# Optimization experiments

Hardware: AMD Instinct MI355X
Metric: run time of the kernel (lower is better)

## Reference

```python
import jax, jax.numpy as jnp
import numpy as np

B, S, E, H = 2, 2048, 1024, 16
D = E // H          # head_dim = 64
HK = H // 4         # heads per kernel group = 4
MASKED_BIAS = -10000.0


def _dwconv_causal(x, w, b):
    # x: [B, h, S, D], w: [D, k], b: [D]; causal depthwise conv along S
    k = w.shape[1]
    s = x.shape[2]
    xp = jnp.pad(x, ((0, 0), (0, 0), (k - 1, 0), (0, 0)))
    out = b
    for i in range(k):
        out = out + xp[:, :, i:i + s, :] * w[:, i]
    return out


def setup_inputs() -> dict:
    key = jax.random.key(0)
    ks = jax.random.split(key, 32)
    inp = {
        'hidden_states': jax.random.normal(ks[0], (B, S, E), jnp.float32),
        'c_attn_w': jax.random.normal(ks[1], (E, 3 * E), jnp.float32) * 0.02,
        'c_attn_b': jnp.zeros((3 * E,), jnp.float32),
        'c_proj_w': jax.random.normal(ks[2], (E, E), jnp.float32) * 0.02,
        'c_proj_b': jnp.zeros((E,), jnp.float32),
    }
    i = 3
    for pre in ('q', 'k', 'v'):
        for kern in (3, 5, 7):
            inp[f'{pre}w{kern}'] = jax.random.normal(ks[i], (D, kern), jnp.float32) * (1.0 / kern)
            inp[f'{pre}b{kern}'] = jnp.zeros((D,), jnp.float32)
            i += 1
    return inp


def _forward(hidden_states, c_attn_w, c_attn_b, c_proj_w, c_proj_b,
             qw3, qb3, qw5, qb5, qw7, qb7,
             kw3, kb3, kw5, kb5, kw7, kb7,
             vw3, vb3, vw5, vb5, vw7, vb7):
    qkv = hidden_states @ c_attn_w + c_attn_b            # [B,S,3E]
    q, k, v = jnp.split(qkv, 3, axis=-1)

    def split_heads(t):
        return t.reshape(B, S, H, D).transpose(0, 2, 1, 3)  # [B,H,S,D]

    q, k, v = split_heads(q), split_heads(k), split_heads(v)

    def tranception_mix(t, ws_bs):
        parts = [t[:, :HK]]
        for g, (w, b) in enumerate(ws_bs):
            parts.append(_dwconv_causal(t[:, (g + 1) * HK:(g + 2) * HK], w, b))
        return jnp.concatenate(parts, axis=1)

    q = tranception_mix(q, [(qw3, qb3), (qw5, qb5), (qw7, qb7)])
    k = tranception_mix(k, [(kw3, kb3), (kw5, kb5), (kw7, kb7)])
    v = tranception_mix(v, [(vw3, vb3), (vw5, vb5), (vw7, vb7)])

    scores = jnp.einsum('bhqd,bhkd->bhqk', q, k) / jnp.sqrt(jnp.float32(D))
    causal = jnp.tril(jnp.ones((S, S), bool))
    scores = jnp.where(causal, scores, jnp.float32(MASKED_BIAS))
    attn = jax.nn.softmax(scores, axis=-1)
    out = jnp.einsum('bhqk,bhkd->bhqd', attn, v)
    out = out.transpose(0, 2, 1, 3).reshape(B, S, E)
    return out @ c_proj_w + c_proj_b


def reference(hidden_states, c_attn_w, c_attn_b, c_proj_w, c_proj_b,
              qw3, qb3, qw5, qb5, qw7, qb7,
              kw3, kb3, kw5, kb5, kw7, kb7,
              vw3, vb3, vw5, vb5, vw7, vb7):
    return _forward(hidden_states, c_attn_w, c_attn_b, c_proj_w, c_proj_b,
                    qw3, qb3, qw5, qb5, qw7, qb7,
                    kw3, kb3, kw5, kb5, kw7, kb7,
                    vw3, vb3, vw5, vb5, vw7, vb7)
```

## Files before the change

### kernel.cpp

```cpp
#include <hip/hip_runtime.h>
#include <stdint.h>
#include <math.h>

typedef unsigned short u16;
typedef __attribute__((ext_vector_type(8))) short short8;
typedef __attribute__((ext_vector_type(4))) float floatx4;

#define DEV static __device__ __forceinline__

struct alignas(8) us4 { u16 x, y, z, w; };
struct alignas(16) us8 { u16 v[8]; };
struct alignas(16) f4 { float x, y, z, w; };
struct alignas(8) f2 { float x, y; };
struct alignas(8) u32x2 { uint32_t x, y; };

DEV u16 f2bf(float f) {
  uint32_t u = __float_as_uint(f);
  u += 0x7fffu + ((u >> 16) & 1u);
  return (u16)(u >> 16);
}
DEV float bf2f(u16 h) { return __uint_as_float(((uint32_t)h) << 16); }

DEV uint32_t pkbf(float a, float b) {
#if __has_builtin(__builtin_amdgcn_cvt_pk_bf16_f32)
  typedef __attribute__((ext_vector_type(2))) __bf16 bf2_t;
  bf2_t v = __builtin_amdgcn_cvt_pk_bf16_f32(a, b);
  uint32_t r; __builtin_memcpy(&r, &v, 4); return r;
#else
  return (uint32_t)f2bf(a) | ((uint32_t)f2bf(b) << 16);
#endif
}

DEV float fexp2(float x) {
#if __has_builtin(__builtin_amdgcn_exp2f)
  return __builtin_amdgcn_exp2f(x);
#else
  return exp2f(x);
#endif
}

DEV void load_lds16(const void* g, void* l) {
  __builtin_amdgcn_global_load_lds((const __attribute__((address_space(1))) void*)g,
                                   (__attribute__((address_space(3))) void*)l, 16, 0, 0);
}

__global__ __launch_bounds__(256) void prep_fused(const float* __restrict__ hidden, u16* __restrict__ h_bf,
                                                  const float* __restrict__ attn_w, u16* __restrict__ wqkvT,
                                                  const float* __restrict__ proj_w, u16* __restrict__ wprojT) {
  __shared__ float tile[32][33];
  const int bx = blockIdx.x;
  const int t = threadIdx.x;
  if (bx < 4096) {
    const int i = (bx * 256 + t) * 4;
    f4 v = *(const f4*)(hidden + i);
    us4 o; o.x = f2bf(v.x); o.y = f2bf(v.y); o.z = f2bf(v.z); o.w = f2bf(v.w);
    *(us4*)(h_bf + i) = o;
    return;
  }
  const float* in; u16* out; int K, N, n0, k0;
  if (bx < 7168) {
    const int bid = bx - 4096;
    in = attn_w; out = wqkvT; K = 1024; N = 3072;
    n0 = (bid % 96) * 32; k0 = (bid / 96) * 32;
  } else {
    const int bid = bx - 7168;
    in = proj_w; out = wprojT; K = 1024; N = 1024;
    n0 = (bid & 31) * 32; k0 = (bid >> 5) * 32;
  }
  const int tx = t & 31, ty = t >> 5;
  for (int i = ty; i < 32; i += 8)
    tile[i][tx] = in[(size_t)(k0 + i) * N + n0 + tx];
  __syncthreads();
  for (int i = ty; i < 32; i += 8)
    out[(size_t)(n0 + i) * K + k0 + tx] = f2bf(tile[tx][i]);
}

template <int EPI, int BN, int NGRP>
__global__ __launch_bounds__(256) void gemm_bt(const u16* __restrict__ A,
                                               const u16* __restrict__ Bt,
                                               const float* __restrict__ bias,
                                               void* __restrict__ outp,
                                               int M, int N, int K) {
  constexpr int NT = BN / 32;
  __shared__ u16 lA[128 * 64];
  __shared__ u16 lB[BN * 64];
  const int t = threadIdx.x;
  const int w = t >> 6, lane = t & 63;
  const int quad = lane >> 4, l15 = lane & 15;
  const int wm = w >> 1, wn = w & 1;
  const int wn_off = wn * (BN / 2);

  const int bid = blockIdx.x;
  const int gsz = 32 * NGRP;
  const int grp = bid / gsz;
  const int r = bid - grp * gsz;
  const int m0 = (r & 31) * 128;
  const int n0 = (grp * NGRP + (r >> 5)) * BN;

  floatx4 acc[4][NT] = {};

  const int srow = t >> 3;
  const int scol = (((t & 7) ^ (srow & 7)) << 3);
  const u16* gA = A + (size_t)(m0 + srow) * K + scol;
  const u16* gB = Bt + (size_t)(n0 + srow) * K + scol;
  u16* sA = lA + t * 8;
  u16* sB = lB + t * 8;
  const size_t rstep = (size_t)32 * K;

  for (int k0 = 0; k0 < K; k0 += 64) {
#pragma unroll
    for (int c = 0; c < 4; c++) load_lds16(gA + c * rstep, sA + c * 2048);
#pragma unroll
    for (int c = 0; c < BN / 32; c++) load_lds16(gB + c * rstep, sB + c * 2048);
    gA += 64; gB += 64;
    __syncthreads();
#pragma unroll
    for (int kc = 0; kc < 2; kc++) {
      short8 af[4], bfr[NT];
#pragma unroll
      for (int mt = 0; mt < 4; mt++)
        af[mt] = *(const short8*)&lA[(wm * 64 + mt * 16 + l15) * 64 + (((kc * 4 + quad) ^ (l15 & 7)) << 3)];
#pragma unroll
      for (int nt = 0; nt < NT; nt++)
        bfr[nt] = *(const short8*)&lB[(wn_off + nt * 16 + l15) * 64 + (((kc * 4 + quad) ^ (l15 & 7)) << 3)];
#pragma unroll
      for (int mt = 0; mt < 4; mt++)
#pragma unroll
        for (int nt = 0; nt < NT; nt++)
          acc[mt][nt] = __builtin_amdgcn_mfma_f32_16x16x32_bf16(bfr[nt], af[mt], acc[mt][nt], 0, 0, 0);
    }
    __syncthreads();
  }

  if (EPI == 0) {
    u16* outq = (u16*)outp;
#pragma unroll
    for (int nt = 0; nt < NT; nt++) {
      const int nb = n0 + wn_off + nt * 16 + quad * 4;
      const f4 bn4 = *(const f4*)&bias[nb];
      const int tensor = nb >> 10, e = nb & 1023;
      const int h = e >> 6, d = e & 63;
      const size_t abase = (size_t)tensor * 4194304 + (size_t)h * 131072 + d;
#pragma unroll
      for (int mt = 0; mt < 4; mt++) {
        const int rr = m0 + wm * 64 + mt * 16 + l15;
        const int b = rr >> 11, s = rr & 2047;
        u32x2 o;
        o.x = pkbf(acc[mt][nt][0] + bn4.x, acc[mt][nt][1] + bn4.y);
        o.y = pkbf(acc[mt][nt][2] + bn4.z, acc[mt][nt][3] + bn4.w);
        *(u32x2*)&outq[abase + (size_t)b * 2097152 + (size_t)s * 64] = o;
      }
    }
  } else {
    float* outf = (float*)outp;
#pragma unroll
    for (int nt = 0; nt < NT; nt++) {
      const int nb = n0 + wn_off + nt * 16 + quad * 4;
      const f4 bn4 = *(const f4*)&bias[nb];
#pragma unroll
      for (int mt = 0; mt < 4; mt++) {
        const int rr = m0 + wm * 64 + mt * 16 + l15;
        f4 o;
        o.x = acc[mt][nt][0] + bn4.x;
        o.y = acc[mt][nt][1] + bn4.y;
        o.z = acc[mt][nt][2] + bn4.z;
        o.w = acc[mt][nt][3] + bn4.w;
        *(f4*)&outf[(size_t)rr * N + nb] = o;
      }
    }
  }
}

struct ConvW { const float* w[9]; const float* b[9]; };

template <int K>
DEV void conv_run(const u16* xt, int sl0, int d, const float* wp, const float* bp,
                  float qscale, float* out32) {
  float wr[K];
#pragma unroll
  for (int j = 0; j < K; j++) wr[j] = wp[d * K + j];
  const float br = bp[d];
  float win[K];
#pragma unroll
  for (int m = 1; m < K; m++) win[m] = bf2f(xt[(sl0 + 6 - K + m) * 68 + d]);
#pragma unroll
  for (int i = 0; i < 32; i++) {
#pragma unroll
    for (int m = 0; m < K - 1; m++) win[m] = win[m + 1];
    win[K - 1] = bf2f(xt[(sl0 + 6 + i) * 68 + d]);
    float val = br;
#pragma unroll
    for (int j = 0; j < K; j++) val += wr[j] * win[j];
    out32[i] = val * qscale;
  }
}

__global__ __launch_bounds__(256) void conv_mix(const u16* __restrict__ qkv, ConvW cw,
                                                u16* __restrict__ qpost,
                                                u16* __restrict__ kpost,
                                                u16* __restrict__ vpostT) {
  __shared__ u16 xt[134 * 68];
  __shared__ u16 yt[64 * 136];
  const int t = threadIdx.x;
  const int s0 = blockIdx.x * 128;
  const int h = blockIdx.y;
  const int tz = blockIdx.z;
  const int tensor = tz >> 1, b = tz & 1;
  const u16* src = qkv + (((size_t)tensor * 2 + b) * 16 + h) * 131072;

  for (int idx = t; idx < 134 * 16; idx += 256) {
    const int row = idx >> 4, c4 = (idx & 15) << 2;
    const int s = s0 - 6 + row;
    us4 v = {0, 0, 0, 0};
    if (s >= 0) v = *(const us4*)&src[(size_t)s * 64 + c4];
    *(us4*)&xt[row * 68 + c4] = v;
  }
  __syncthreads();

  const int group = h >> 2;
  const float* wp = (group > 0) ? cw.w[tensor * 3 + group - 1] : nullptr;
  const float* bp = (group > 0) ? cw.b[tensor * 3 + group - 1] : nullptr;
  const float qscale = (tensor == 0) ? 0.18033688f : 1.0f;

  const int d = t & 63;
  const int sl0 = (t >> 6) * 32;

  float out32[32];
  if (group == 0) {
#pragma unroll
    for (int i = 0; i < 32; i++)
      out32[i] = bf2f(xt[(sl0 + 6 + i) * 68 + d]) * qscale;
  } else if (group == 1) {
    conv_run<3>(xt, sl0, d, wp, bp, qscale, out32);
  } else if (group == 2) {
    conv_run<5>(xt, sl0, d, wp, bp, qscale, out32);
  } else {
    conv_run<7>(xt, sl0, d, wp, bp, qscale, out32);
  }

  if (tensor < 2) {
    u16* outp = (tensor == 0) ? qpost : kpost;
    const size_t ob = (((size_t)b * 16 + h) * 2048 + s0) * 64;
#pragma unroll
    for (int i = 0; i < 32; i++)
      outp[ob + (size_t)(sl0 + i) * 64 + d] = f2bf(out32[i]);
  } else {
#pragma unroll
    for (int i = 0; i < 32; i++)
      yt[d * 136 + sl0 + i] = f2bf(out32[i]);
    __syncthreads();
    const size_t ob = ((size_t)b * 16 + h) * 64;
    const int sl = (t & 15) * 8;
#pragma unroll
    for (int pass = 0; pass < 4; pass++) {
      const int dd = (t >> 4) + pass * 16;
      us8 vv = *(const us8*)&yt[dd * 136 + sl];
      *(us8*)&vpostT[(ob + dd) * 2048 + s0 + sl] = vv;
    }
  }
}

static __device__ const unsigned char kOrder[24] = {
  7, 8, 10, 12, 14, 16, 18, 20, 22, 23,
  6, 21, 5, 19, 4, 17, 3, 15, 2, 13, 1, 11, 0, 9
};

__global__ __launch_bounds__(256) void attn_fwd(const u16* __restrict__ Q,
                                                const u16* __restrict__ Kp,
                                                const u16* __restrict__ Vt,
                                                u16* __restrict__ Out,
                                                u16* __restrict__ Opart,
                                                float* __restrict__ lpart) {
  __shared__ u16 lK[2][128 * 64];
  __shared__ u16 lV[2][64 * 128];
  __shared__ u16 lP[4][32 * 64];
  const int t = threadIdx.x;
  const int w = t >> 6, lane = t & 63;
  const int quad = lane >> 4, l15 = lane & 15;
  const int e7 = l15 & 7;

  const int lin = blockIdx.x;
  const int xcd = lin & 7;
  const int rest = lin >> 3;
  const int grp = rest / 24;
  const int slot = kOrder[rest - grp * 24];
  const int bh = grp * 8 + xcd;

  int qi, jbeg, jend, split, half;
  if (slot < 8) {
    qi = slot; jbeg = 0; jend = qi + 1; split = 0; half = 0;
  } else {
    const int k = slot - 8;
    qi = 8 + (k >> 1); half = k & 1;
    jbeg = half ? 8 : 0; jend = half ? qi + 1 : 8; split = 1;
  }

  const int b = bh >> 4, h = bh & 15;
  const size_t qkbase = (size_t)bh * 131072;
  const int qblk = qi * 128 + w * 32;

  const int krow = t >> 3;
  const int kcol = (((t & 7) ^ (krow & 7)) << 3);
  const u16* gK = Kp + qkbase + (size_t)krow * 64 + kcol;
  const int vrow = t >> 4;
  const int vcol = (((t & 15) ^ vrow) << 3);
  const u16* gV = Vt + qkbase + (size_t)vrow * 2048 + vcol;
  u16* myP = lP[w];

  short8 qf[2][2];
#pragma unroll
  for (int qt = 0; qt < 2; qt++)
#pragma unroll
    for (int kc = 0; kc < 2; kc++)
      qf[qt][kc] = *(const short8*)&Q[qkbase + (size_t)(qblk + qt * 16 + l15) * 64 + kc * 32 + quad * 8];

  {
    const int j0 = jbeg * 128;
    u16* sK = &lK[0][0] + t * 8;
    u16* sV = &lV[0][0] + t * 8;
#pragma unroll
    for (int c = 0; c < 4; c++) {
      load_lds16(gK + (size_t)(j0 + c * 32) * 64, sK + c * 2048);
      load_lds16(gV + j0 + c * 16 * 2048, sV + c * 2048);
    }
  }
  asm volatile("s_waitcnt vmcnt(0)" ::: "memory");
  __builtin_amdgcn_s_barrier();

  float lst[2] = {0.0f, 0.0f};
  floatx4 accO[4][2] = {};

  for (int j = jbeg; j < jend; ++j) {
    const int cur = (j - jbeg) & 1;

    if (j + 1 < jend) {
      const int j0n = (j + 1) * 128;
      u16* sK = &lK[cur ^ 1][0] + t * 8;
      u16* sV = &lV[cur ^ 1][0] + t * 8;
#pragma unroll
      for (int c = 0; c < 4; c++) {
        load_lds16(gK + (size_t)(j0n + c * 32) * 64, sK + c * 2048);
        load_lds16(gV + j0n + c * 16 * 2048, sV + c * 2048);
      }
    }

    const int j0 = j * 128;
    const u16* cK = lK[cur];
    const u16* cV = lV[cur];

    floatx4 accS[8][2] = {};
    __builtin_amdgcn_s_setprio(1);
#pragma unroll
    for (int kvt = 0; kvt < 8; kvt++) {
#pragma unroll
      for (int kc = 0; kc < 2; kc++) {
        const short8 a = *(const short8*)&cK[(kvt * 16 + l15) * 64 + (((kc * 4 + quad) ^ e7) << 3)];
#pragma unroll
        for (int qt = 0; qt < 2; qt++)
          accS[kvt][qt] = __builtin_amdgcn_mfma_f32_16x16x32_bf16(a, qf[qt][kc], accS[kvt][qt], 0, 0, 0);
      }
    }
    __builtin_amdgcn_s_setprio(0);

    if (j == qi) {
#pragma unroll
      for (int qt = 0; qt < 2; qt++) {
        const int q = qblk + qt * 16 + l15;
#pragma unroll
        for (int kvt = 0; kvt < 8; kvt++)
#pragma unroll
          for (int r = 0; r < 4; r++) {
            const int kv = j0 + kvt * 16 + quad * 4 + r;
            if (kv > q) accS[kvt][qt][r] = -3.0e38f;
          }
      }
    }

    uint32_t pk01[2][8], pk23[2][8];
#pragma unroll
    for (int qt = 0; qt < 2; qt++) {
      float ts = 0.0f;
#pragma unroll
      for (int kvt = 0; kvt < 8; kvt++) {
        const float p0 = fexp2(accS[kvt][qt][0]);
        const float p1 = fexp2(accS[kvt][qt][1]);
        const float p2 = fexp2(accS[kvt][qt][2]);
        const float p3 = fexp2(accS[kvt][qt][3]);
        ts += (p0 + p1) + (p2 + p3);
        pk01[qt][kvt] = pkbf(p0, p1);
        pk23[qt][kvt] = pkbf(p2, p3);
      }
      lst[qt] += ts;
    }

#pragma unroll
    for (int kvh = 0; kvh < 2; kvh++) {
#pragma unroll
      for (int qt = 0; qt < 2; qt++) {
        const int prow = (qt * 16 + l15) * 64;
#pragma unroll
        for (int kt = 0; kt < 4; kt++) {
          const int kvt = kvh * 4 + kt;
          const int slotp = (kt * 2 + (quad >> 1)) ^ e7;
          u32x2 pk; pk.x = pk01[qt][kvt]; pk.y = pk23[qt][kvt];
          *(u32x2*)&myP[prow + slotp * 8 + (quad & 1) * 4] = pk;
        }
      }
      asm volatile("s_waitcnt lgkmcnt(0)" ::: "memory");
      __builtin_amdgcn_s_setprio(1);
#pragma unroll
      for (int kk = 0; kk < 2; kk++) {
        const int kvc = kvh * 2 + kk;
        short8 pf[2];
#pragma unroll
        for (int qt = 0; qt < 2; qt++)
          pf[qt] = *(const short8*)&myP[(qt * 16 + l15) * 64 + (((kk * 4 + quad) ^ e7) << 3)];
#pragma unroll
        for (int dt = 0; dt < 4; dt++) {
          const short8 vf = *(const short8*)&cV[(dt * 16 + l15) * 128 + (((kvc * 4 + quad) ^ l15) << 3)];
#pragma unroll
          for (int qt = 0; qt < 2; qt++)
            accO[dt][qt] = __builtin_amdgcn_mfma_f32_16x16x32_bf16(vf, pf[qt], accO[dt][qt], 0, 0, 0);
        }
      }
      __builtin_amdgcn_s_setprio(0);
    }

    if (j + 1 < jend) {
      asm volatile("s_waitcnt vmcnt(0)" ::: "memory");
      __builtin_amdgcn_s_barrier();
    }
  }

#pragma unroll
  for (int qt = 0; qt < 2; qt++) {
    lst[qt] += __shfl_xor(lst[qt], 16);
    lst[qt] += __shfl_xor(lst[qt], 32);
  }

  if (!split) {
#pragma unroll
    for (int qt = 0; qt < 2; qt++) {
      const float inv = 1.0f / lst[qt];
      const int q = qblk + qt * 16 + l15;
#pragma unroll
      for (int dt = 0; dt < 4; dt++) {
        u32x2 o;
        o.x = pkbf(accO[dt][qt][0] * inv, accO[dt][qt][1] * inv);
        o.y = pkbf(accO[dt][qt][2] * inv, accO[dt][qt][3] * inv);
        *(u32x2*)&Out[((size_t)b * 2048 + q) * 1024 + h * 64 + dt * 16 + quad * 4] = o;
      }
    }
  } else {
    const int pidx = (bh * 8 + (qi - 8)) * 2 + half;
    u16* op = Opart + (size_t)pidx * 8192;
#pragma unroll
    for (int qt = 0; qt < 2; qt++) {
      const int ql = w * 32 + qt * 16 + l15;
#pragma unroll
      for (int dt = 0; dt < 4; dt++) {
        u32x2 o;
        o.x = pkbf(accO[dt][qt][0], accO[dt][qt][1]);
        o.y = pkbf(accO[dt][qt][2], accO[dt][qt][3]);
        *(u32x2*)&op[(size_t)ql * 64 + dt * 16 + quad * 4] = o;
      }
      if (quad == 0) lpart[pidx * 128 + ql] = lst[qt];
    }
  }
}

__global__ __launch_bounds__(256) void attn_reduce(const u16* __restrict__ Opart,
                                                   const float* __restrict__ lpart,
                                                   u16* __restrict__ Out) {
  const int qr = blockIdx.x;
  const int bh = blockIdx.y;
  const int b = bh >> 4, h = bh & 15;
  const int t = threadIdx.x;
  const int row = t >> 1, dh = (t & 1) * 32;
  const int pbase = (bh * 8 + qr) * 2;

  const float l1 = lpart[pbase * 128 + row];
  const float l2 = lpart[(pbase + 1) * 128 + row];
  const float inv = 1.0f / (l1 + l2);

  const u16* s1 = Opart + ((size_t)pbase * 128 + row) * 64 + dh;
  const u16* s2 = Opart + ((size_t)(pbase + 1) * 128 + row) * 64 + dh;
  u16* dst = Out + ((size_t)b * 2048 + (8 + qr) * 128 + row) * 1024 + h * 64 + dh;
#pragma unroll
  for (int i = 0; i < 4; i++) {
    us8 v1 = *(const us8*)&s1[i * 8];
    us8 v2 = *(const us8*)&s2[i * 8];
    float o[8];
#pragma unroll
    for (int e = 0; e < 8; e++) o[e] = (bf2f(v1.v[e]) + bf2f(v2.v[e])) * inv;
    us4 a, c;
    uint32_t w0 = pkbf(o[0], o[1]), w1 = pkbf(o[2], o[3]);
    uint32_t w2 = pkbf(o[4], o[5]), w3 = pkbf(o[6], o[7]);
    u32x2 lo; lo.x = w0; lo.y = w1;
    u32x2 hi; hi.x = w2; hi.y = w3;
    *(u32x2*)&dst[i * 8] = lo;
    *(u32x2*)&dst[i * 8 + 4] = hi;
    (void)a; (void)c;
  }
}

extern "C" void kernel_launch(void* const* d_in, const int* in_sizes, int n_in,
                              void* d_out, int out_size, void* d_ws, size_t ws_size,
                              hipStream_t stream) {
  (void)in_sizes; (void)n_in; (void)out_size; (void)ws_size;
  const float* hidden = (const float*)d_in[0];
  const float* attn_w = (const float*)d_in[1];
  const float* attn_b = (const float*)d_in[2];
  const float* proj_w = (const float*)d_in[3];
  const float* proj_b = (const float*)d_in[4];
  ConvW cw;
  for (int i = 0; i < 9; i++) {
    cw.w[i] = (const float*)d_in[5 + 2 * i];
    cw.b[i] = (const float*)d_in[6 + 2 * i];
  }

  uint8_t* ws = (uint8_t*)d_ws;
  u16* h_bf   = (u16*)(ws + 0);
  u16* wqkvT  = (u16*)(ws + 8388608);
  u16* qkvpre = (u16*)(ws + 14680064);
  u16* qpost  = (u16*)(ws + 39845888);
  u16* kpost  = (u16*)(ws + 48234496);
  u16* vpostT = (u16*)(ws + 56623104);
  u16* attno  = (u16*)(ws + 65011712);
  u16* wprojT = (u16*)(ws + 73400320);
  u16* Opart  = (u16*)(ws + 0);
  float* lpart = (float*)(ws + 8388608);

  prep_fused<<<8192, 256, 0, stream>>>(hidden, h_bf, attn_w, wqkvT, proj_w, wprojT);
  gemm_bt<0, 128, 6><<<768, 256, 0, stream>>>(h_bf, wqkvT, attn_b, (void*)qkvpre, 4096, 3072, 1024);
  conv_mix<<<dim3(16, 16, 6), 256, 0, stream>>>(qkvpre, cw, qpost, kpost, vpostT);
  attn_fwd<<<dim3(768), 256, 0, stream>>>(qpost, kpost, vpostT, attno, Opart, lpart);
  attn_reduce<<<dim3(8, 32), 256, 0, stream>>>(Opart, lpart, attno);
  gemm_bt<1, 64, 8><<<512, 256, 0, stream>>>(attno, wprojT, proj_b, d_out, 4096, 1024, 1024);
}
```

Before: 242.7 us.

## Load V fragments directly from global into registers instead of LDS staging

The attention kernel no longer stages V tiles through double-buffered shared memory. Each wave reads its V MFMA operands straight from global memory into registers in two halves, and vmcnt waits let the second half and the next K prefetch overlap with softmax and the first PV MFMAs. The barrier moves to the top of the loop, and the block-to-work mapping changes from a divide to shift/mask indexing. This cuts LDS footprint and LDS traffic, which may raise occupancy, at the cost of redundant uncoalesced global V reads per wave and more live registers.

Result: slower. 255.4 us (+5.2%).

```diff
diff --git a/kernel.cpp b/kernel.cpp
--- a/kernel.cpp
+++ b/kernel.cpp
@@ -272,7 +272,6 @@
                                                 u16* __restrict__ Opart,
                                                 float* __restrict__ lpart) {
   __shared__ u16 lK[2][128 * 64];
-  __shared__ u16 lV[2][64 * 128];
   __shared__ u16 lP[4][32 * 64];
   const int t = threadIdx.x;
   const int w = t >> 6, lane = t & 63;
@@ -282,8 +281,8 @@
   const int lin = blockIdx.x;
   const int xcd = lin & 7;
   const int rest = lin >> 3;
-  const int grp = rest / 24;
-  const int slot = kOrder[rest - grp * 24];
+  const int grp = rest & 3;
+  const int slot = kOrder[rest >> 2];
   const int bh = grp * 8 + xcd;
 
   int qi, jbeg, jend, split, half;
@@ -302,9 +301,7 @@
   const int krow = t >> 3;
   const int kcol = (((t & 7) ^ (krow & 7)) << 3);
   const u16* gK = Kp + qkbase + (size_t)krow * 64 + kcol;
-  const int vrow = t >> 4;
-  const int vcol = (((t & 15) ^ vrow) << 3);
-  const u16* gV = Vt + qkbase + (size_t)vrow * 2048 + vcol;
+  const u16* pV = Vt + qkbase + (size_t)l15 * 2048 + quad * 8;
   u16* myP = lP[w];
 
   short8 qf[2][2];
@@ -313,16 +310,13 @@
 #pragma unroll
     for (int kc = 0; kc < 2; kc++)
       qf[qt][kc] = *(const short8*)&Q[qkbase + (size_t)(qblk + qt * 16 + l15) * 64 + kc * 32 + quad * 8];
+  asm volatile("" ::: "memory");
 
   {
     const int j0 = jbeg * 128;
     u16* sK = &lK[0][0] + t * 8;
-    u16* sV = &lV[0][0] + t * 8;
-#pragma unroll
-    for (int c = 0; c < 4; c++) {
-      load_lds16(gK + (size_t)(j0 + c * 32) * 64, sK + c * 2048);
-      load_lds16(gV + j0 + c * 16 * 2048, sV + c * 2048);
-    }
+#pragma unroll
+    for (int c = 0; c < 4; c++) load_lds16(gK + (size_t)(j0 + c * 32) * 64, sK + c * 2048);
   }
   asm volatile("s_waitcnt vmcnt(0)" ::: "memory");
   __builtin_amdgcn_s_barrier();
@@ -332,35 +326,40 @@
 
   for (int j = jbeg; j < jend; ++j) {
     const int cur = (j - jbeg) & 1;
+    const int j0 = j * 128;
+    const u16* cK = lK[cur];
+
+    if (j > jbeg) __builtin_amdgcn_s_barrier();
+
+    floatx4 accS[8][2] = {};
+    __builtin_amdgcn_s_setprio(1);
+#pragma unroll
+    for (int kvt = 0; kvt < 8; kvt++) {
+#pragma unroll
+      for (int kc = 0; kc < 2; kc++) {
+        const short8 a = *(const short8*)&cK[(kvt * 16 + l15) * 64 + (((kc * 4 + quad) ^ e7) << 3)];
+#pragma unroll
+        for (int qt = 0; qt < 2; qt++)
+          accS[kvt][qt] = __builtin_amdgcn_mfma_f32_16x16x32_bf16(a, qf[qt][kc], accS[kvt][qt], 0, 0, 0);
+      }
+    }
+    __builtin_amdgcn_s_setprio(0);
+
+    short8 vfr0[2][4];
+#pragma unroll
+    for (int kk = 0; kk < 2; kk++)
+#pragma unroll
+      for (int dt = 0; dt < 4; dt++)
+        vfr0[kk][dt] = *(const short8*)&pV[(size_t)(dt * 16) * 2048 + j0 + kk * 32];
+    asm volatile("" ::: "memory");
 
     if (j + 1 < jend) {
       const int j0n = (j + 1) * 128;
       u16* sK = &lK[cur ^ 1][0] + t * 8;
-      u16* sV = &lV[cur ^ 1][0] + t * 8;
-#pragma unroll
-      for (int c = 0; c < 4; c++) {
-        load_lds16(gK + (size_t)(j0n + c * 32) * 64, sK + c * 2048);
-        load_lds16(gV + j0n + c * 16 * 2048, sV + c * 2048);
-      }
-    }
-
-    const int j0 = j * 128;
-    const u16* cK = lK[cur];
-    const u16* cV = lV[cur];
-
-    floatx4 accS[8][2] = {};
-    __builtin_amdgcn_s_setprio(1);
-#pragma unroll
-    for (int kvt = 0; kvt < 8; kvt++) {
-#pragma unroll
-      for (int kc = 0; kc < 2; kc++) {
-        const short8 a = *(const short8*)&cK[(kvt * 16 + l15) * 64 + (((kc * 4 + quad) ^ e7) << 3)];
-#pragma unroll
-        for (int qt = 0; qt < 2; qt++)
-          accS[kvt][qt] = __builtin_amdgcn_mfma_f32_16x16x32_bf16(a, qf[qt][kc], accS[kvt][qt], 0, 0, 0);
-      }
-    }
-    __builtin_amdgcn_s_setprio(0);
+#pragma unroll
+      for (int c = 0; c < 4; c++) load_lds16(gK + (size_t)(j0n + c * 32) * 64, sK + c * 2048);
+    }
+    asm volatile("" ::: "memory");
 
     if (j == qi) {
 #pragma unroll
@@ -393,43 +392,70 @@
       lst[qt] += ts;
     }
 
-#pragma unroll
-    for (int kvh = 0; kvh < 2; kvh++) {
-#pragma unroll
-      for (int qt = 0; qt < 2; qt++) {
-        const int prow = (qt * 16 + l15) * 64;
-#pragma unroll
-        for (int kt = 0; kt < 4; kt++) {
-          const int kvt = kvh * 4 + kt;
-          const int slotp = (kt * 2 + (quad >> 1)) ^ e7;
-          u32x2 pk; pk.x = pk01[qt][kvt]; pk.y = pk23[qt][kvt];
-          *(u32x2*)&myP[prow + slotp * 8 + (quad & 1) * 4] = pk;
-        }
-      }
-      asm volatile("s_waitcnt lgkmcnt(0)" ::: "memory");
-      __builtin_amdgcn_s_setprio(1);
-#pragma unroll
-      for (int kk = 0; kk < 2; kk++) {
-        const int kvc = kvh * 2 + kk;
-        short8 pf[2];
+    if (j + 1 < jend) asm volatile("s_waitcnt vmcnt(4)" ::: "memory");
+    else              asm volatile("s_waitcnt vmcnt(0)" ::: "memory");
+
+    short8 vfr1[2][4];
+#pragma unroll
+    for (int kk = 0; kk < 2; kk++)
+#pragma unroll
+      for (int dt = 0; dt < 4; dt++)
+        vfr1[kk][dt] = *(const short8*)&pV[(size_t)(dt * 16) * 2048 + j0 + (2 + kk) * 32];
+    asm volatile("" ::: "memory");
+
+#pragma unroll
+    for (int qt = 0; qt < 2; qt++) {
+      const int prow = (qt * 16 + l15) * 64;
+#pragma unroll
+      for (int kt = 0; kt < 4; kt++) {
+        const int slotp = (kt * 2 + (quad >> 1)) ^ e7;
+        u32x2 pk; pk.x = pk01[qt][kt]; pk.y = pk23[qt][kt];
+        *(u32x2*)&myP[prow + slotp * 8 + (quad & 1) * 4] = pk;
+      }
+    }
+    asm volatile("s_waitcnt lgkmcnt(0)" ::: "memory");
+    __builtin_amdgcn_s_setprio(1);
+#pragma unroll
+    for (int kk = 0; kk < 2; kk++) {
+      short8 pf[2];
+#pragma unroll
+      for (int qt = 0; qt < 2; qt++)
+        pf[qt] = *(const short8*)&myP[(qt * 16 + l15) * 64 + (((kk * 4 + quad) ^ e7) << 3)];
+#pragma unroll
+      for (int dt = 0; dt < 4; dt++)
 #pragma unroll
         for (int qt = 0; qt < 2; qt++)
-          pf[qt] = *(const short8*)&myP[(qt * 16 + l15) * 64 + (((kk * 4 + quad) ^ e7) << 3)];
-#pragma unroll
-        for (int dt = 0; dt < 4; dt++) {
-          const short8 vf = *(const short8*)&cV[(dt * 16 + l15) * 128 + (((kvc * 4 + quad) ^ l15) << 3)];
-#pragma unroll
-          for (int qt = 0; qt < 2; qt++)
-            accO[dt][qt] = __builtin_amdgcn_mfma_f32_16x16x32_bf16(vf, pf[qt], accO[dt][qt], 0, 0, 0);
-        }
-      }
-      __builtin_amdgcn_s_setprio(0);
-    }
-
-    if (j + 1 < jend) {
-      asm volatile("s_waitcnt vmcnt(0)" ::: "memory");
-      __builtin_amdgcn_s_barrier();
-    }
+          accO[dt][qt] = __builtin_amdgcn_mfma_f32_16x16x32_bf16(vfr0[kk][dt], pf[qt], accO[dt][qt], 0, 0, 0);
+    }
+    __builtin_amdgcn_s_setprio(0);
+
+    asm volatile("s_waitcnt vmcnt(0)" ::: "memory");
+
+#pragma unroll
+    for (int qt = 0; qt < 2; qt++) {
+      const int prow = (qt * 16 + l15) * 64;
+#pragma unroll
+      for (int kt = 0; kt < 4; kt++) {
+        const int slotp = (kt * 2 + (quad >> 1)) ^ e7;
+        u32x2 pk; pk.x = pk01[qt][4 + kt]; pk.y = pk23[qt][4 + kt];
+        *(u32x2*)&myP[prow + slotp * 8 + (quad & 1) * 4] = pk;
+      }
+    }
+    asm volatile("s_waitcnt lgkmcnt(0)" ::: "memory");
+    __builtin_amdgcn_s_setprio(1);
+#pragma unroll
+    for (int kk = 0; kk < 2; kk++) {
+      short8 pf[2];
+#pragma unroll
+      for (int qt = 0; qt < 2; qt++)
+        pf[qt] = *(const short8*)&myP[(qt * 16 + l15) * 64 + (((kk * 4 + quad) ^ e7) << 3)];
+#pragma unroll
+      for (int dt = 0; dt < 4; dt++)
+#pragma unroll
+        for (int qt = 0; qt < 2; qt++)
+          accO[dt][qt] = __builtin_amdgcn_mfma_f32_16x16x32_bf16(vfr1[kk][dt], pf[qt], accO[dt][qt], 0, 0, 0);
+    }
+    __builtin_amdgcn_s_setprio(0);
   }
 
 #pragma unroll
@@ -493,14 +519,10 @@
     float o[8];
 #pragma unroll
     for (int e = 0; e < 8; e++) o[e] = (bf2f(v1.v[e]) + bf2f(v2.v[e])) * inv;
-    us4 a, c;
-    uint32_t w0 = pkbf(o[0], o[1]), w1 = pkbf(o[2], o[3]);
-    uint32_t w2 = pkbf(o[4], o[5]), w3 = pkbf(o[6], o[7]);
-    u32x2 lo; lo.x = w0; lo.y = w1;
-    u32x2 hi; hi.x = w2; hi.y = w3;
+    u32x2 lo; lo.x = pkbf(o[0], o[1]); lo.y = pkbf(o[2], o[3]);
+    u32x2 hi; hi.x = pkbf(o[4], o[5]); hi.y = pkbf(o[6], o[7]);
     *(u32x2*)&dst[i * 8] = lo;
     *(u32x2*)&dst[i * 8 + 4] = hi;
-    (void)a; (void)c;
   }
 }
 
```
